# Optimization experiments

Hardware: AMD Instinct MI355X
Metric: run time of the kernel (lower is better)

The kernel has to match this reference:

```python
import jax, jax.numpy as jnp
import numpy as np

N_NODES = 50000


def graph_conv(x, W, b, src, dst, n_nodes):
    # DGL GraphConv with norm='both': h = D_in^{-1/2} A D_out^{-1/2} x W + b
    ones = jnp.ones(src.shape[0], dtype=x.dtype)
    deg_out = jax.ops.segment_sum(ones, src, num_segments=n_nodes)
    deg_in = jax.ops.segment_sum(ones, dst, num_segments=n_nodes)
    norm_out = jnp.power(jnp.clip(deg_out, 1.0, None), -0.5)
    norm_in = jnp.power(jnp.clip(deg_in, 1.0, None), -0.5)
    x = x * norm_out[:, None]
    msgs = x[src]                                   # [E, d] gather
    agg = jax.ops.segment_sum(msgs, dst, num_segments=n_nodes)  # [N, d] scatter-add
    agg = agg * norm_in[:, None]
    return agg @ W + b


def setup_inputs() -> dict:
    key = jax.random.key(0)
    ks = jax.random.split(key, 16)
    d = 128
    h = 2 * d
    od = 64
    E = 800000
    T = 4096

    def lin(k, fan_in, fan_out):
        bound = 1.0 / np.sqrt(fan_in)
        k1, k2 = jax.random.split(k)
        W = jax.random.uniform(k1, (fan_in, fan_out), jnp.float32, -bound, bound)
        b = jax.random.uniform(k2, (fan_out,), jnp.float32, -bound, bound)
        return W, b

    features = jax.random.normal(ks[0], (N_NODES, d), jnp.float32)
    src = jax.random.randint(ks[1], (E,), 0, N_NODES)
    dst = jax.random.randint(ks[2], (E,), 0, N_NODES)
    trigger_nodes = jax.random.randint(ks[3], (T,), 0, N_NODES)

    W1, b1 = lin(ks[4], d, h)
    W2, b2 = lin(ks[5], h, d)
    Wf, bf = lin(ks[6], d, d)
    Wf1, bf1 = lin(ks[7], d, d)
    We, be = lin(ks[8], d, od)
    We1, be1 = lin(ks[9], od, od)

    return {
        "features": features, "src": src, "dst": dst,
        "trigger_nodes": trigger_nodes,
        "W1": W1, "b1": b1, "W2": W2, "b2": b2,
        "Wf": Wf, "bf": bf, "Wf1": Wf1, "bf1": bf1,
        "We": We, "be": be, "We1": We1, "be1": be1,
    }


def reference(features, src, dst, trigger_nodes,
              W1, b1, W2, b2, Wf, bf, Wf1, bf1, We, be, We1, be1):
    n = features.shape[0]
    h = jax.nn.relu(graph_conv(features, W1, b1, src, dst, n))   # [N, 2d]
    h = jax.nn.relu(graph_conv(h, W2, b2, src, dst, n))          # [N, d]
    ht = h[trigger_nodes]                                        # [T, d] gather
    feat = jax.nn.relu(ht @ Wf + bf) @ Wf1 + bf1                 # [T, d]
    edge_weight = jax.nn.relu(ht @ We + be) @ We1 + be1          # [T, od]
    return (feat, edge_weight)
```

## Files before the change

### kernel.cpp

```cpp
#include <hip/hip_runtime.h>
#include <hip/hip_bf16.h>


typedef __attribute__((ext_vector_type(8))) short short8;
typedef __attribute__((ext_vector_type(4))) float f32x4;

#define NHALF_CAP 25088

union U16B { uint4 u; short8 s; };

__device__ __forceinline__ unsigned pack_hl(float v)
{
    unsigned u = __builtin_bit_cast(unsigned, v);
    unsigned rb = u + 0x7fffu + ((u >> 16) & 1u);
    float hf = __builtin_bit_cast(float, rb & 0xffff0000u);
    float r = v - hf;
    unsigned l = __builtin_bit_cast(unsigned, r) & 0xffff0000u;
    return (rb >> 16) | l;
}

__device__ __forceinline__ float decode_hl(unsigned u)
{
    float hf = __builtin_bit_cast(float, u << 16);
    float lf = __builtin_bit_cast(float, u & 0xffff0000u);
    return hf + lf;
}

__device__ __forceinline__ void unpack_hl(uint4 a, uint4 b, short8& h, short8& l)
{
    U16B H, L;
    H.u.x = (a.x & 0xffffu) | (a.y << 16);
    H.u.y = (a.z & 0xffffu) | (a.w << 16);
    H.u.z = (b.x & 0xffffu) | (b.y << 16);
    H.u.w = (b.z & 0xffffu) | (b.w << 16);
    L.u.x = (a.x >> 16) | (a.y & 0xffff0000u);
    L.u.y = (a.z >> 16) | (a.w & 0xffff0000u);
    L.u.z = (b.x >> 16) | (b.y & 0xffff0000u);
    L.u.w = (b.z >> 16) | (b.w & 0xffff0000u);
    h = H.s; l = L.s;
}

__global__ __launch_bounds__(256) void hist_kernel(
    const int* __restrict__ src, const int* __restrict__ dst,
    unsigned* __restrict__ part_in, unsigned* __restrict__ part_out,
    int E, int chunk, int nhalf)
{
    __shared__ unsigned c32[NHALF_CAP];
    const int b = blockIdx.x;
    const int* __restrict__ idx = blockIdx.y ? src : dst;
    unsigned* __restrict__ part = blockIdx.y ? part_out : part_in;

    for (int i = threadIdx.x; i < nhalf; i += 256) c32[i] = 0u;
    __syncthreads();

    const int base = b * chunk;
    const int lim = min(base + chunk, E);
    for (int e = base + threadIdx.x; e < lim; e += 256) {
        int n = idx[e];
        atomicAdd(&c32[n >> 1], (n & 1) ? 0x10000u : 1u);
    }
    __syncthreads();

    unsigned* __restrict__ o = part + (long)b * nhalf;
    for (int i = threadIdx.x; i < nhalf; i += 256) o[i] = c32[i];
}

__global__ __launch_bounds__(256) void merge_kernel(
    unsigned* __restrict__ part_in, const unsigned* __restrict__ part_out,
    int* __restrict__ deg_in, float* __restrict__ norm_in,
    float* __restrict__ norm_out, int nhalf, int N)
{
    __shared__ unsigned gsum[4][64];
    const int il = threadIdx.x & 63;
    const int bg = threadIdx.x >> 6;
    const int i = blockIdx.x * 64 + il;
    const bool valid = (i < nhalf);

    unsigned p[32];
    unsigned run = 0u;
    if (valid) {
        #pragma unroll
        for (int j = 0; j < 32; ++j)
            p[j] = part_in[(long)(bg * 32 + j) * nhalf + i];
        #pragma unroll
        for (int j = 0; j < 32; ++j) run += p[j];
    }
    gsum[bg][il] = run;
    __syncthreads();

    unsigned base = 0u;
    #pragma unroll
    for (int g = 0; g < 4; ++g) {
        unsigned v = gsum[g][il];
        if (g < bg) base += v;
    }

    unsigned ro = 0u;
    if (valid) {
        #pragma unroll
        for (int j = 0; j < 32; ++j)
            ro += part_out[(long)(bg * 32 + j) * nhalf + i];
    }

    if (valid) {
        unsigned acc = base;
        #pragma unroll
        for (int j = 0; j < 32; ++j) {
            part_in[(long)(bg * 32 + j) * nhalf + i] = acc;
            acc += p[j];
        }
        if (bg == 3) {
            int n0 = 2 * i, n1 = 2 * i + 1;
            int d0 = (int)(acc & 0xffffu), d1 = (int)(acc >> 16);
            deg_in[n0] = d0;
            norm_in[n0] = rsqrtf(fmaxf((float)d0, 1.0f));
            if (n1 < N) {
                deg_in[n1] = d1;
                norm_in[n1] = rsqrtf(fmaxf((float)d1, 1.0f));
            }
        }
    }

    __syncthreads();
    gsum[bg][il] = ro;
    __syncthreads();
    if (valid && bg == 0) {
        unsigned rt = gsum[0][il] + gsum[1][il] + gsum[2][il] + gsum[3][il];
        int n0 = 2 * i, n1 = 2 * i + 1;
        norm_out[n0] = rsqrtf(fmaxf((float)(rt & 0xffffu), 1.0f));
        if (n1 < N)
            norm_out[n1] = rsqrtf(fmaxf((float)(rt >> 16), 1.0f));
    }
}

__global__ __launch_bounds__(256) void scan1_kernel(
    const int* __restrict__ deg, int* __restrict__ rowptr,
    int* __restrict__ bsum, int N)
{
    __shared__ int s[256];
    int t = threadIdx.x;
    int i = blockIdx.x * 256 + t;
    s[t] = (i < N) ? deg[i] : 0;
    __syncthreads();
    #pragma unroll
    for (int off = 1; off < 256; off <<= 1) {
        int v = (t >= off) ? s[t - off] : 0;
        __syncthreads();
        s[t] += v;
        __syncthreads();
    }
    if (i < N) rowptr[i + 1] = s[t];
    if (t == 255) bsum[blockIdx.x] = s[255];
}

__global__ __launch_bounds__(256) void scan2_kernel(int* __restrict__ bsum, int nb)
{
    __shared__ int s[256];
    int t = threadIdx.x;
    s[t] = (t < nb) ? bsum[t] : 0;
    __syncthreads();
    #pragma unroll
    for (int off = 1; off < 256; off <<= 1) {
        int v = (t >= off) ? s[t - off] : 0;
        __syncthreads();
        s[t] += v;
        __syncthreads();
    }
    if (t < nb) bsum[t] = s[t];
}

__global__ __launch_bounds__(256) void scan3_kernel(
    int* __restrict__ rowptr, const int* __restrict__ bsum, int N)
{
    int b = blockIdx.x;
    int i = b * 256 + threadIdx.x;
    if (i < N) {
        int add = (b > 0) ? bsum[b - 1] : 0;
        rowptr[i + 1] += add;
    }
    if (i == 0) rowptr[0] = 0;
}

__global__ __launch_bounds__(256) void fill2_kernel(
    const int* __restrict__ src, const int* __restrict__ dst,
    const int* __restrict__ rowptr, const unsigned* __restrict__ part_in,
    int* __restrict__ ecol, int E, int chunk, int nhalf)
{
    __shared__ unsigned c32[NHALF_CAP];
    const int b = blockIdx.x;
    const unsigned* __restrict__ pref = part_in + (long)b * nhalf;
    for (int i = threadIdx.x; i < nhalf; i += 256) c32[i] = pref[i];
    __syncthreads();

    const int base = b * chunk;
    const int lim = min(base + chunk, E);
    for (int e = base + threadIdx.x; e < lim; e += 256) {
        int r = dst[e];
        unsigned old = atomicAdd(&c32[r >> 1], (r & 1) ? 0x10000u : 1u);
        unsigned slot = (r & 1) ? (old >> 16) : (old & 0xffffu);
        ecol[rowptr[r] + (int)slot] = src[e];
    }
}

struct WPrep {
    const float* w[6];
    unsigned* o[6];
    int K[6], N[6], base[7];
};

__global__ __launch_bounds__(256) void wprep_kernel(WPrep p)
{
    int t = blockIdx.x * 256 + threadIdx.x;
    if (t >= p.base[6]) return;
    int s = 0;
    while (t >= p.base[s + 1]) ++s;
    int loc = t - p.base[s];
    int K = p.K[s], N = p.N[s];
    int n = loc / K, k = loc - n * K;
    p.o[s][(long)n * K + k] = pack_hl(p.w[s][(long)k * N + n]);
}

__global__ __launch_bounds__(256) void gather4_kernel(
    const float* __restrict__ x, const float* __restrict__ nsrc,
    const int* __restrict__ rowptr, const int* __restrict__ ecol,
    unsigned* __restrict__ out, int N)
{
    const int wave = threadIdx.x >> 6;
    const int lane = threadIdx.x & 63;
    const int r = blockIdx.x * 4 + wave;
    if (r >= N) return;
    const int q = lane & 31;
    const int h = lane >> 5;
    const int beg = rowptr[r], end = rowptr[r + 1];
    const float4* __restrict__ x4 = (const float4*)x;

    float4 acc = make_float4(0.f, 0.f, 0.f, 0.f);
    int k = beg + h;
    int sA = (k < end) ? ecol[k] : -1;
    int sB = (k + 2 < end) ? ecol[k + 2] : -1;
    float4 vA = make_float4(0.f, 0.f, 0.f, 0.f), vB = vA;
    float nA = 0.f, nB = 0.f;
    if (sA >= 0) { vA = x4[(long)sA * 32 + q]; nA = nsrc[sA]; }
    if (sB >= 0) { vB = x4[(long)sB * 32 + q]; nB = nsrc[sB]; }
    while (sA >= 0) {
        int sC = (k + 4 < end) ? ecol[k + 4] : -1;
        float4 vC = make_float4(0.f, 0.f, 0.f, 0.f);
        float nC = 0.f;
        if (sC >= 0) { vC = x4[(long)sC * 32 + q]; nC = nsrc[sC]; }
        acc.x = fmaf(vA.x, nA, acc.x);
        acc.y = fmaf(vA.y, nA, acc.y);
        acc.z = fmaf(vA.z, nA, acc.z);
        acc.w = fmaf(vA.w, nA, acc.w);
        sA = sB; vA = vB; nA = nB;
        sB = sC; vB = vC; nB = nC;
        k += 2;
    }
    acc.x += __shfl(acc.x, lane ^ 32);
    acc.y += __shfl(acc.y, lane ^ 32);
    acc.z += __shfl(acc.z, lane ^ 32);
    acc.w += __shfl(acc.w, lane ^ 32);
    if (h == 0) {
        uint4 o;
        o.x = pack_hl(acc.x); o.y = pack_hl(acc.y);
        o.z = pack_hl(acc.z); o.w = pack_hl(acc.w);
        *reinterpret_cast<uint4*>(&out[(long)r * 128 + q * 4]) = o;
    }
}

__global__ __launch_bounds__(256) void gather_trig256_kernel(
    const unsigned* __restrict__ h1s, const int* __restrict__ trig,
    const float* __restrict__ norm_in,
    const int* __restrict__ rowptr, const int* __restrict__ ecol,
    unsigned* __restrict__ agg2ts, int T)
{
    const int wave = threadIdx.x >> 6;
    const int lane = threadIdx.x & 63;
    const int b = blockIdx.x * 4 + wave;
    if (b >= T) return;
    const int r = trig[b];
    const int beg = rowptr[r], end = rowptr[r + 1];
    const uint4* __restrict__ h4 = (const uint4*)h1s;

    float4 acc = make_float4(0.f, 0.f, 0.f, 0.f);
    int k = beg;
    int sA = (k < end) ? ecol[k] : -1;
    int sB = (k + 1 < end) ? ecol[k + 1] : -1;
    uint4 vA = make_uint4(0u, 0u, 0u, 0u), vB = vA;
    if (sA >= 0) vA = h4[(long)sA * 64 + lane];
    if (sB >= 0) vB = h4[(long)sB * 64 + lane];
    while (sA >= 0) {
        int sC = (k + 2 < end) ? ecol[k + 2] : -1;
        uint4 vC = make_uint4(0u, 0u, 0u, 0u);
        if (sC >= 0) vC = h4[(long)sC * 64 + lane];
        acc.x += decode_hl(vA.x);
        acc.y += decode_hl(vA.y);
        acc.z += decode_hl(vA.z);
        acc.w += decode_hl(vA.w);
        sA = sB; vA = vB;
        sB = sC; vB = vC;
        ++k;
    }
    const float ni = norm_in[r];
    uint4 o;
    o.x = pack_hl(acc.x * ni); o.y = pack_hl(acc.y * ni);
    o.z = pack_hl(acc.z * ni); o.w = pack_hl(acc.w * ni);
    *reinterpret_cast<uint4*>(&agg2ts[(long)b * 256 + lane * 4]) = o;
}

__global__ __launch_bounds__(256) void mgemm256_kernel(
    const unsigned* __restrict__ A, const unsigned* __restrict__ Bp,
    const float* __restrict__ bias, const float* __restrict__ ni,
    const float* __restrict__ no, unsigned* __restrict__ Cp, int M)
{
    constexpr int K = 128;
    const int tid = threadIdx.x;
    const int lane = tid & 63, wave = tid >> 6;
    const int l15 = lane & 15, l4 = lane >> 4;
    const int row0 = blockIdx.x * 128;

    long aof[2];
    #pragma unroll
    for (int i = 0; i < 2; ++i) {
        int r = row0 + wave * 32 + i * 16 + l15;
        if (r > M - 1) r = M - 1;
        aof[i] = (long)r * K + l4 * 8;
    }
    const long bbase = (long)l15 * K + l4 * 8;

    uint4 abuf[2][2][2];
    #pragma unroll
    for (int i = 0; i < 2; ++i) {
        abuf[0][i][0] = *reinterpret_cast<const uint4*>(&A[aof[i] + 0]);
        abuf[0][i][1] = *reinterpret_cast<const uint4*>(&A[aof[i] + 4]);
        abuf[1][i][0] = *reinterpret_cast<const uint4*>(&A[aof[i] + 32]);
        abuf[1][i][1] = *reinterpret_cast<const uint4*>(&A[aof[i] + 36]);
    }

    f32x4 acc[2][16];
    #pragma unroll
    for (int i = 0; i < 2; ++i)
        #pragma unroll
        for (int j = 0; j < 16; ++j)
            acc[i][j] = (f32x4){0.f, 0.f, 0.f, 0.f};

    short8 ah[2], al[2];
    uint4 b0 = *reinterpret_cast<const uint4*>(&Bp[bbase]);
    uint4 b1 = *reinterpret_cast<const uint4*>(&Bp[bbase + 4]);

    #pragma unroll
    for (int t = 0; t < 64; ++t) {
        const int c = t >> 4, j = t & 15;
        if (j == 0) {
            const int cp = c & 1;
            unpack_hl(abuf[cp][0][0], abuf[cp][0][1], ah[0], al[0]);
            unpack_hl(abuf[cp][1][0], abuf[cp][1][1], ah[1], al[1]);
            if (c + 2 < 4) {
                #pragma unroll
                for (int i = 0; i < 2; ++i) {
                    abuf[cp][i][0] = *reinterpret_cast<const uint4*>(&A[aof[i] + (c + 2) * 32]);
                    abuf[cp][i][1] = *reinterpret_cast<const uint4*>(&A[aof[i] + (c + 2) * 32 + 4]);
                }
            }
        }
        uint4 nb0, nb1;
        if (t + 1 < 64) {
            const int c1 = (t + 1) >> 4, j1 = (t + 1) & 15;
            const long na = bbase + (long)j1 * 16 * K + c1 * 32;
            nb0 = *reinterpret_cast<const uint4*>(&Bp[na]);
            nb1 = *reinterpret_cast<const uint4*>(&Bp[na + 4]);
        }
        short8 bh, bl;
        unpack_hl(b0, b1, bh, bl);
        #pragma unroll
        for (int i = 0; i < 2; ++i) {
            acc[i][j] = __builtin_amdgcn_mfma_f32_16x16x32_bf16(ah[i], bh, acc[i][j], 0, 0, 0);
            acc[i][j] = __builtin_amdgcn_mfma_f32_16x16x32_bf16(ah[i], bl, acc[i][j], 0, 0, 0);
            acc[i][j] = __builtin_amdgcn_mfma_f32_16x16x32_bf16(al[i], bh, acc[i][j], 0, 0, 0);
        }
        b0 = nb0; b1 = nb1;
    }

    #pragma unroll
    for (int i = 0; i < 2; ++i) {
        const int rbase = row0 + wave * 32 + i * 16 + l4 * 4;
        #pragma unroll
        for (int g = 0; g < 4; ++g) {
            const int row = rbase + g;
            if (row >= M) continue;
            const float niv = ni[row], nov = no[row];
            #pragma unroll
            for (int j = 0; j < 16; ++j) {
                const int col = j * 16 + l15;
                float v = fmaxf(fmaf(niv, acc[i][j][g], bias[col]), 0.f) * nov;
                Cp[(long)row * 256 + col] = pack_hl(v);
            }
        }
    }
}

template<int TN, bool RELU, bool PACK_OUT>
__global__ __launch_bounds__(256) void mgemm_kernel(
    const unsigned* __restrict__ A, const unsigned* __restrict__ Bp,
    const float* __restrict__ bias, const float* __restrict__ rowscale,
    const float* __restrict__ outscale,
    float* __restrict__ C, unsigned* __restrict__ Cp, int M, int N, int K)
{
    constexpr int IM = 2, KC = 32, TM = 128;
    constexpr int JF = TN / 16;
    constexpr int BLD = (TN * KC) / (4 * 256);

    __shared__ unsigned sB[KC * TN];

    const int tid = threadIdx.x;
    const int lane = tid & 63;
    const int wave = tid >> 6;
    const int l15 = lane & 15, l4 = lane >> 4;
    const int row0 = blockIdx.y * TM;
    const int col0 = blockIdx.x * TN;

    int bro[BLD], bgr[BLD];
    long bof[BLD];
    #pragma unroll
    for (int l = 0; l < BLD; ++l) {
        int idx = tid + 256 * l;
        bro[l] = idx % TN;
        bgr[l] = idx / TN;
        bof[l] = (long)(col0 + bro[l]) * K + bgr[l] * 4;
    }
    long aof[IM];
    #pragma unroll
    for (int i = 0; i < IM; ++i) {
        int r = row0 + wave * 32 + i * 16 + l15;
        if (r > M - 1) r = M - 1;
        aof[i] = (long)r * K + l4 * 8;
    }

    uint4 cB[BLD], nB[BLD], cA[IM][2], nA[IM][2];
    #pragma unroll
    for (int l = 0; l < BLD; ++l)
        cB[l] = *reinterpret_cast<const uint4*>(&Bp[bof[l]]);
    #pragma unroll
    for (int i = 0; i < IM; ++i) {
        cA[i][0] = *reinterpret_cast<const uint4*>(&A[aof[i]]);
        cA[i][1] = *reinterpret_cast<const uint4*>(&A[aof[i] + 4]);
    }

    f32x4 acc[IM][JF];
    #pragma unroll
    for (int i = 0; i < IM; ++i)
        #pragma unroll
        for (int j = 0; j < JF; ++j)
            acc[i][j] = (f32x4){0.f, 0.f, 0.f, 0.f};

    const int nc = K / KC;
    for (int c = 0; c < nc; ++c) {
        #pragma unroll
        for (int l = 0; l < BLD; ++l)
            *reinterpret_cast<uint4*>(&sB[(bgr[l] * TN + bro[l]) * 4]) = cB[l];
        __syncthreads();

        if (c + 1 < nc) {
            const int kc = (c + 1) * KC;
            #pragma unroll
            for (int l = 0; l < BLD; ++l)
                nB[l] = *reinterpret_cast<const uint4*>(&Bp[bof[l] + kc]);
            #pragma unroll
            for (int i = 0; i < IM; ++i) {
                nA[i][0] = *reinterpret_cast<const uint4*>(&A[aof[i] + kc]);
                nA[i][1] = *reinterpret_cast<const uint4*>(&A[aof[i] + kc + 4]);
            }
        }

        short8 ah[IM], al[IM];
        #pragma unroll
        for (int i = 0; i < IM; ++i)
            unpack_hl(cA[i][0], cA[i][1], ah[i], al[i]);

        #pragma unroll
        for (int j = 0; j < JF; ++j) {
            const int rowb = j * 16 + l15;
            uint4 b0 = *reinterpret_cast<const uint4*>(&sB[((2 * l4 + 0) * TN + rowb) * 4]);
            uint4 b1 = *reinterpret_cast<const uint4*>(&sB[((2 * l4 + 1) * TN + rowb) * 4]);
            short8 bh, bl;
            unpack_hl(b0, b1, bh, bl);
            #pragma unroll
            for (int i = 0; i < IM; ++i) {
                acc[i][j] = __builtin_amdgcn_mfma_f32_16x16x32_bf16(ah[i], bh, acc[i][j], 0, 0, 0);
                acc[i][j] = __builtin_amdgcn_mfma_f32_16x16x32_bf16(ah[i], bl, acc[i][j], 0, 0, 0);
                acc[i][j] = __builtin_amdgcn_mfma_f32_16x16x32_bf16(al[i], bh, acc[i][j], 0, 0, 0);
            }
        }
        __syncthreads();

        if (c + 1 < nc) {
            #pragma unroll
            for (int l = 0; l < BLD; ++l) cB[l] = nB[l];
            #pragma unroll
            for (int i = 0; i < IM; ++i) { cA[i][0] = nA[i][0]; cA[i][1] = nA[i][1]; }
        }
    }

    #pragma unroll
    for (int i = 0; i < IM; ++i) {
        const int rb = row0 + wave * 32 + i * 16 + l4 * 4;
        #pragma unroll
        for (int j = 0; j < JF; ++j) {
            const int col = col0 + j * 16 + l15;
            const float bs = bias ? bias[col] : 0.0f;
            #pragma unroll
            for (int g = 0; g < 4; ++g) {
                const int row = rb + g;
                if (row >= M) continue;
                float v = acc[i][j][g];
                if (rowscale) v *= rowscale[row];
                v += bs;
                if (RELU) v = fmaxf(v, 0.0f);
                if (outscale) v *= outscale[row];
                if (PACK_OUT) Cp[(long)row * N + col] = pack_hl(v);
                else          C[(long)row * N + col] = v;
            }
        }
    }
}

static inline long align8(long x) { return (x + 7) & ~7L; }

extern "C" void kernel_launch(void* const* d_in, const int* in_sizes, int n_in,
                              void* d_out, int out_size, void* d_ws, size_t ws_size,
                              hipStream_t stream)
{
    const float* features = (const float*)d_in[0];
    const int*   src      = (const int*)d_in[1];
    const int*   dst      = (const int*)d_in[2];
    const int*   trig     = (const int*)d_in[3];
    const float* W1  = (const float*)d_in[4];
    const float* b1  = (const float*)d_in[5];
    const float* W2  = (const float*)d_in[6];
    const float* b2  = (const float*)d_in[7];
    const float* Wf  = (const float*)d_in[8];
    const float* bf  = (const float*)d_in[9];
    const float* Wf1 = (const float*)d_in[10];
    const float* bf1 = (const float*)d_in[11];
    const float* We  = (const float*)d_in[12];
    const float* be  = (const float*)d_in[13];
    const float* We1 = (const float*)d_in[14];
    const float* be1 = (const float*)d_in[15];

    const int  d   = 128, h2d = 256, od = 64;
    const int  N   = in_sizes[0] / d;
    const int  E   = in_sizes[1];
    const int  T   = in_sizes[3];
    const int  NB  = (N + 255) / 256;

    const int  HB    = 128;
    const int  chunk = (E + HB - 1) / HB;
    const int  nhalf = (N + 1) / 2;

    char* wsb = (char*)d_ws;
    long off = 0;
    auto takeF = [&](long n) { float* p = (float*)(wsb + off); off += align8(n) * 4; return p; };
    auto takeI = [&](long n) { int*   p = (int*)  (wsb + off); off += align8(n) * 4; return p; };
    auto takeU = [&](long n) { unsigned* p = (unsigned*)(wsb + off); off += align8(n) * 4; return p; };

    float*    norm_out = takeF(N);
    float*    norm_in  = takeF(N);
    int*      deg_in   = takeI(N);
    int*      rowptr   = takeI(N + 1);
    int*      bsum     = takeI(256);
    int*      ecol     = takeI(E);
    unsigned* part_in  = takeU((long)HB * nhalf);
    unsigned* part_out = takeU((long)HB * nhalf);
    unsigned* agg1     = takeU((long)N * d);
    unsigned* h1s      = takeU((long)N * h2d);
    unsigned* agg2ts   = takeU((long)T * h2d);
    unsigned* h2t      = takeU((long)T * d);
    unsigned* tmpf     = takeU((long)T * d);
    unsigned* tmpe     = takeU((long)T * od);
    unsigned* w1p      = takeU((long)h2d * d);
    unsigned* w2p      = takeU((long)d * h2d);
    unsigned* wfp      = takeU((long)d * d);
    unsigned* wf1p     = takeU((long)d * d);
    unsigned* wep      = takeU((long)od * d);
    unsigned* we1p     = takeU((long)od * od);

    float* out_feat = (float*)d_out;
    float* out_edge = out_feat + (long)T * d;

    WPrep wp;
    wp.w[0] = W1;  wp.o[0] = w1p;  wp.K[0] = d;   wp.N[0] = h2d;
    wp.w[1] = W2;  wp.o[1] = w2p;  wp.K[1] = h2d; wp.N[1] = d;
    wp.w[2] = Wf;  wp.o[2] = wfp;  wp.K[2] = d;   wp.N[2] = d;
    wp.w[3] = Wf1; wp.o[3] = wf1p; wp.K[3] = d;   wp.N[3] = d;
    wp.w[4] = We;  wp.o[4] = wep;  wp.K[4] = d;   wp.N[4] = od;
    wp.w[5] = We1; wp.o[5] = we1p; wp.K[5] = od;  wp.N[5] = od;
    wp.base[0] = 0;
    for (int i = 0; i < 6; ++i) wp.base[i + 1] = wp.base[i] + wp.K[i] * wp.N[i];
    wprep_kernel<<<dim3((wp.base[6] + 255) / 256), dim3(256), 0, stream>>>(wp);

    hist_kernel<<<dim3(HB, 2), dim3(256), 0, stream>>>(
        src, dst, part_in, part_out, E, chunk, nhalf);
    merge_kernel<<<dim3((nhalf + 63) / 64), dim3(256), 0, stream>>>(
        part_in, part_out, deg_in, norm_in, norm_out, nhalf, N);
    scan1_kernel<<<dim3(NB), dim3(256), 0, stream>>>(deg_in, rowptr, bsum, N);
    scan2_kernel<<<dim3(1), dim3(256), 0, stream>>>(bsum, NB);
    scan3_kernel<<<dim3(NB), dim3(256), 0, stream>>>(rowptr, bsum, N);
    fill2_kernel<<<dim3(HB), dim3(256), 0, stream>>>(
        src, dst, rowptr, part_in, ecol, E, chunk, nhalf);

    const int GY = (N + 127) / 128;
    const int GT = T / 128;

    gather4_kernel<<<dim3((N + 3) / 4), dim3(256), 0, stream>>>(
        features, norm_out, rowptr, ecol, agg1, N);
    mgemm256_kernel<<<dim3(GY), dim3(256), 0, stream>>>(
        agg1, w1p, b1, norm_in, norm_out, h1s, N);

    gather_trig256_kernel<<<dim3((T + 3) / 4), dim3(256), 0, stream>>>(
        h1s, trig, norm_in, rowptr, ecol, agg2ts, T);
    mgemm_kernel<64, true, true><<<dim3(d / 64, GT), dim3(256), 0, stream>>>(
        agg2ts, w2p, b2, nullptr, nullptr, nullptr, h2t, T, d, h2d);

    mgemm_kernel<64, true, true><<<dim3(d / 64, GT), dim3(256), 0, stream>>>(
        h2t, wfp, bf, nullptr, nullptr, nullptr, tmpf, T, d, d);
    mgemm_kernel<64, false, false><<<dim3(d / 64, GT), dim3(256), 0, stream>>>(
        tmpf, wf1p, bf1, nullptr, nullptr, out_feat, nullptr, T, d, d);

    mgemm_kernel<64, true, true><<<dim3(od / 64, GT), dim3(256), 0, stream>>>(
        h2t, wep, be, nullptr, nullptr, nullptr, tmpe, T, od, d);
    mgemm_kernel<64, false, false><<<dim3(od / 64, GT), dim3(256), 0, stream>>>(
        tmpe, we1p, be1, nullptr, nullptr, out_edge, nullptr, T, od, od);
}
```

Baseline: 281.6 us.

## Split feature dimension into 8 slices per block in SpMM gather kernels

Both CSR gather kernels now split the feature row into 8 column slices, each handled by a separate block, while more lanes within a wave walk different edges in parallel (16 edges at once for layer 1, 8 for the trigger gather), followed by a shuffle reduction. This raises edge-level parallelism and memory-level parallelism for rows with modest degree, and removes the explicit software prefetch pipeline. In exchange each source row is fetched as 64- or 128-byte pieces by 8 different blocks, the edge index list is re-read 8 times, and there is extra shuffle-reduction overhead.

Result: slower. 337.9 us (+20.0%).

```diff
diff --git a/kernel.cpp b/kernel.cpp
--- a/kernel.cpp
+++ b/kernel.cpp
@@ -220,91 +220,96 @@
     p.o[s][(long)n * K + k] = pack_hl(p.w[s][(long)k * N + n]);
 }
 
-__global__ __launch_bounds__(256) void gather4_kernel(
+__global__ __launch_bounds__(256) void gather4s_kernel(
     const float* __restrict__ x, const float* __restrict__ nsrc,
     const int* __restrict__ rowptr, const int* __restrict__ ecol,
     unsigned* __restrict__ out, int N)
 {
+    const int slice = blockIdx.x & 7;
+    const int rb = blockIdx.x >> 3;
     const int wave = threadIdx.x >> 6;
     const int lane = threadIdx.x & 63;
-    const int r = blockIdx.x * 4 + wave;
+    const int r = rb * 4 + wave;
     if (r >= N) return;
-    const int q = lane & 31;
-    const int h = lane >> 5;
+    const int q = lane & 3;
+    const int h = lane >> 2;
     const int beg = rowptr[r], end = rowptr[r + 1];
     const float4* __restrict__ x4 = (const float4*)x;
 
     float4 acc = make_float4(0.f, 0.f, 0.f, 0.f);
     int k = beg + h;
     int sA = (k < end) ? ecol[k] : -1;
-    int sB = (k + 2 < end) ? ecol[k + 2] : -1;
-    float4 vA = make_float4(0.f, 0.f, 0.f, 0.f), vB = vA;
-    float nA = 0.f, nB = 0.f;
-    if (sA >= 0) { vA = x4[(long)sA * 32 + q]; nA = nsrc[sA]; }
-    if (sB >= 0) { vB = x4[(long)sB * 32 + q]; nB = nsrc[sB]; }
     while (sA >= 0) {
-        int sC = (k + 4 < end) ? ecol[k + 4] : -1;
-        float4 vC = make_float4(0.f, 0.f, 0.f, 0.f);
-        float nC = 0.f;
-        if (sC >= 0) { vC = x4[(long)sC * 32 + q]; nC = nsrc[sC]; }
-        acc.x = fmaf(vA.x, nA, acc.x);
-        acc.y = fmaf(vA.y, nA, acc.y);
-        acc.z = fmaf(vA.z, nA, acc.z);
-        acc.w = fmaf(vA.w, nA, acc.w);
-        sA = sB; vA = vB; nA = nB;
-        sB = sC; vB = vC; nB = nC;
-        k += 2;
-    }
-    acc.x += __shfl(acc.x, lane ^ 32);
-    acc.y += __shfl(acc.y, lane ^ 32);
-    acc.z += __shfl(acc.z, lane ^ 32);
-    acc.w += __shfl(acc.w, lane ^ 32);
+        int sB = (k + 16 < end) ? ecol[k + 16] : -1;
+        float ns = nsrc[sA];
+        float4 v = x4[(long)sA * 32 + slice * 4 + q];
+        acc.x = fmaf(v.x, ns, acc.x);
+        acc.y = fmaf(v.y, ns, acc.y);
+        acc.z = fmaf(v.z, ns, acc.z);
+        acc.w = fmaf(v.w, ns, acc.w);
+        sA = sB;
+        k += 16;
+    }
+    #pragma unroll
+    for (int m = 4; m <= 32; m <<= 1) {
+        acc.x += __shfl(acc.x, lane ^ m);
+        acc.y += __shfl(acc.y, lane ^ m);
+        acc.z += __shfl(acc.z, lane ^ m);
+        acc.w += __shfl(acc.w, lane ^ m);
+    }
     if (h == 0) {
         uint4 o;
         o.x = pack_hl(acc.x); o.y = pack_hl(acc.y);
         o.z = pack_hl(acc.z); o.w = pack_hl(acc.w);
-        *reinterpret_cast<uint4*>(&out[(long)r * 128 + q * 4]) = o;
-    }
-}
-
-__global__ __launch_bounds__(256) void gather_trig256_kernel(
+        *reinterpret_cast<uint4*>(&out[(long)r * 128 + slice * 16 + q * 4]) = o;
+    }
+}
+
+__global__ __launch_bounds__(256) void gather_trig256s_kernel(
     const unsigned* __restrict__ h1s, const int* __restrict__ trig,
     const float* __restrict__ norm_in,
     const int* __restrict__ rowptr, const int* __restrict__ ecol,
     unsigned* __restrict__ agg2ts, int T)
 {
+    const int slice = blockIdx.x & 7;
+    const int bb = blockIdx.x >> 3;
     const int wave = threadIdx.x >> 6;
     const int lane = threadIdx.x & 63;
-    const int b = blockIdx.x * 4 + wave;
+    const int b = bb * 4 + wave;
     if (b >= T) return;
+    const int q = lane & 7;
+    const int h = lane >> 3;
     const int r = trig[b];
     const int beg = rowptr[r], end = rowptr[r + 1];
     const uint4* __restrict__ h4 = (const uint4*)h1s;
 
     float4 acc = make_float4(0.f, 0.f, 0.f, 0.f);
-    int k = beg;
+    int k = beg + h;
     int sA = (k < end) ? ecol[k] : -1;
-    int sB = (k + 1 < end) ? ecol[k + 1] : -1;
-    uint4 vA = make_uint4(0u, 0u, 0u, 0u), vB = vA;
-    if (sA >= 0) vA = h4[(long)sA * 64 + lane];
-    if (sB >= 0) vB = h4[(long)sB * 64 + lane];
     while (sA >= 0) {
-        int sC = (k + 2 < end) ? ecol[k + 2] : -1;
-        uint4 vC = make_uint4(0u, 0u, 0u, 0u);
-        if (sC >= 0) vC = h4[(long)sC * 64 + lane];
-        acc.x += decode_hl(vA.x);
-        acc.y += decode_hl(vA.y);
-        acc.z += decode_hl(vA.z);
-        acc.w += decode_hl(vA.w);
-        sA = sB; vA = vB;
-        sB = sC; vB = vC;
-        ++k;
-    }
-    const float ni = norm_in[r];
-    uint4 o;
-    o.x = pack_hl(acc.x * ni); o.y = pack_hl(acc.y * ni);
-    o.z = pack_hl(acc.z * ni); o.w = pack_hl(acc.w * ni);
-    *reinterpret_cast<uint4*>(&agg2ts[(long)b * 256 + lane * 4]) = o;
+        int sB = (k + 8 < end) ? ecol[k + 8] : -1;
+        uint4 v = h4[(long)sA * 64 + slice * 8 + q];
+        acc.x += decode_hl(v.x);
+        acc.y += decode_hl(v.y);
+        acc.z += decode_hl(v.z);
+        acc.w += decode_hl(v.w);
+        sA = sB;
+        k += 8;
+    }
+    #pragma unroll
+    for (int m = 8; m <= 32; m <<= 1) {
+        acc.x += __shfl(acc.x, lane ^ m);
+        acc.y += __shfl(acc.y, lane ^ m);
+        acc.z += __shfl(acc.z, lane ^ m);
+        acc.w += __shfl(acc.w, lane ^ m);
+    }
+    if (h == 0) {
+        const float ni = norm_in[r];
+        uint4 o;
+        o.x = pack_hl(acc.x * ni); o.y = pack_hl(acc.y * ni);
+        o.z = pack_hl(acc.z * ni); o.w = pack_hl(acc.w * ni);
+        *reinterpret_cast<uint4*>(&agg2ts[(long)b * 256 + slice * 32 + q * 4]) = o;
+    }
 }
 
 __global__ __launch_bounds__(256) void mgemm256_kernel(
@@ -610,12 +615,12 @@
     const int GY = (N + 127) / 128;
     const int GT = T / 128;
 
-    gather4_kernel<<<dim3((N + 3) / 4), dim3(256), 0, stream>>>(
+    gather4s_kernel<<<dim3(((N + 3) / 4) * 8), dim3(256), 0, stream>>>(
         features, norm_out, rowptr, ecol, agg1, N);
     mgemm256_kernel<<<dim3(GY), dim3(256), 0, stream>>>(
         agg1, w1p, b1, norm_in, norm_out, h1s, N);
 
-    gather_trig256_kernel<<<dim3((T + 3) / 4), dim3(256), 0, stream>>>(
+    gather_trig256s_kernel<<<dim3(((T + 3) / 4) * 8), dim3(256), 0, stream>>>(
         h1s, trig, norm_in, rowptr, ecol, agg2ts, T);
     mgemm_kernel<64, true, true><<<dim3(d / 64, GT), dim3(256), 0, stream>>>(
         agg2ts, w2p, b2, nullptr, nullptr, nullptr, h2t, T, d, h2d);
```
